# Performance work log

Measured on AMD Instinct MI355X. Metric: run time of the kernel, lower is better.

## Reference

```python
import jax, jax.numpy as jnp
import numpy as np

B, N, C = 2, 2048, 1152
H = 16
HD = C // H  # 72
SCALE = HD ** -0.5
NEG = -100000000.0  # -1e8 bias for fp32 masked positions


def setup_inputs() -> dict:
    key = jax.random.key(0)
    k1, k2, k3, k4, k5 = jax.random.split(key, 5)
    x = jax.random.normal(k1, (B, N, C), dtype=jnp.float32)
    attn_mask = jax.random.randint(k2, (B, N), 0, 2, dtype=jnp.int32)
    w_qkv = jax.random.normal(k3, (3 * C, C), dtype=jnp.float32) * 0.02
    w_proj = jax.random.normal(k4, (C, C), dtype=jnp.float32) * 0.02
    b_proj = jax.random.normal(k5, (C,), dtype=jnp.float32) * 0.02
    return {"x": x, "attn_mask": attn_mask, "w_qkv": w_qkv, "w_proj": w_proj, "b_proj": b_proj}


def reference(x, attn_mask, w_qkv, w_proj, b_proj):
    # qkv projection: [B,N,3C] -> [3,B,H,N,HD]
    qkv = (x @ w_qkv.T).reshape(B, N, 3, H, HD).transpose(2, 0, 3, 1, 4)
    q, k, v = qkv[0], qkv[1], qkv[2]

    # additive mask bias from outer product of per-token 0/1 mask
    m = attn_mask.astype(x.dtype)          # [B,N]
    mm = m[:, :, None] * m[:, None, :]      # [B,N,N]
    bias = jnp.where(mm == 0, NEG, jnp.where(mm == 1, 0.0, mm))
    bias = bias[:, None, :, :]              # [B,1,N,N] broadcast over heads

    # math-branch attention: full QK^T, bias add, softmax, NaN patch, AV
    attn = jnp.einsum('bhqd,bhkd->bhqk', q, k) * SCALE + bias
    attn = jax.nn.softmax(attn, axis=-1)
    attn = jnp.where(jnp.isnan(attn), 0.0, attn)
    out = jnp.einsum('bhqk,bhkd->bqhd', attn, v).reshape(B, N, C)

    return out @ w_proj.T + b_proj
```

## Files before the change

### kernel.cpp

```cpp
#include <hip/hip_runtime.h>

#define B_   2
#define N_   2048
#define C_   1152
#define H_   16
#define HD_  72
#define QKV_W 3456
#define SCALE_ 0.11785113019775793f
#define NEG_  -100000000.0f
#define HDP  96
#define HDV  80
#define PRE_  0.1700219068852255f
#define FMAX_ 4.0f
#define KNEG_ 16384.0f

typedef __bf16    bf16x8 __attribute__((ext_vector_type(8)));
typedef _Float16  f16x8  __attribute__((ext_vector_type(8)));
typedef _Float16  f16x4  __attribute__((ext_vector_type(4)));
typedef float     f32x4  __attribute__((ext_vector_type(4)));

#define GLOAD_LDS16(gp, lp)                                                    \
  __builtin_amdgcn_global_load_lds(                                            \
      (const __attribute__((address_space(1))) void*)(gp),                     \
      (__attribute__((address_space(3))) void*)(lp), 16, 0, 0)

static __device__ __forceinline__ unsigned pack2h(_Float16 a, _Float16 b) {
  union { _Float16 h[2]; unsigned u; } u;
  u.h[0] = a; u.h[1] = b; return u.u;
}

__global__ __launch_bounds__(256)
void split3_f16(const float* __restrict__ x, const float* __restrict__ wq,
                const float* __restrict__ wp,
                _Float16* __restrict__ xf, _Float16* __restrict__ wqf,
                _Float16* __restrict__ wpf,
                float* __restrict__ meanAcc, int nmv,
                int n8x, int n8q, int n8p) {
  int i = blockIdx.x * 256 + threadIdx.x;
  if (i < nmv) meanAcc[i] = 0.0f;
  const float* src; _Float16* dst;
  if (i < n8x) { src = x; dst = xf; }
  else if (i < n8x + n8q) { i -= n8x; src = wq; dst = wqf; }
  else {
    i -= n8x + n8q;
    if (i >= n8p) return;
    src = wp; dst = wpf;
  }
  const float4* p = (const float4*)src + (size_t)i * 2;
  float4 a = p[0], b = p[1];
  float xs[8] = {a.x, a.y, a.z, a.w, b.x, b.y, b.z, b.w};
  f16x8 hv;
#pragma unroll
  for (int r = 0; r < 8; ++r) hv[r] = (_Float16)xs[r];
  *(f16x8*)(dst + (size_t)i * 8) = hv;
}

__global__ __launch_bounds__(256)
void gemm_f16(const _Float16* __restrict__ A, const _Float16* __restrict__ Bm,
              const float* __restrict__ bias, float* __restrict__ Cout,
              int M, int Nn, int K) {
  __shared__ uint4 lds[2][1024];

  const int tid  = threadIdx.x;
  const int wv   = tid >> 6;
  const int lane = tid & 63;
  const int wm   = wv >> 1;
  const int wn   = wv & 1;
  const int m0 = blockIdx.x * 128, n0 = blockIdx.y * 128;

  const char* gp[4];
  int gd[4];
#pragma unroll
  for (int i = 0; i < 4; ++i) {
    const int gid = wv * 4 + i;
    if (gid < 8) {
      gd[i] = gid * 64;
      gp[i] = (const char*)(A + (size_t)(m0 + gid * 16 + (lane & 15)) * K +
                            ((lane >> 4) << 3));
    } else {
      const int g2 = gid - 8;
      gd[i] = 512 + g2 * 64;
      gp[i] = (const char*)(Bm + (size_t)(n0 + g2 * 16 + (lane & 15)) * K +
                            ((lane >> 4) << 3));
    }
  }

#pragma unroll
  for (int i = 0; i < 4; ++i) {
    GLOAD_LDS16(gp[i], &lds[0][gd[i]]);
    gp[i] += 64;
  }

  f32x4 acc[4][4] = {};
  const int nk = K >> 5;

  for (int kt = 0; kt < nk; ++kt) {
    const int cur = kt & 1, nxt = cur ^ 1;
    __syncthreads();

    if (kt < nk - 1) {
#pragma unroll
      for (int i = 0; i < 4; ++i) {
        GLOAD_LDS16(gp[i], &lds[nxt][gd[i]]);
        gp[i] += 64;
      }
    }

    const uint4* cbuf = lds[cur];
    f16x8 af[4], bf[4];
#pragma unroll
    for (int t = 0; t < 4; ++t) {
      af[t] = *(const f16x8*)&cbuf[(wm * 4 + t) * 64 + lane];
      bf[t] = *(const f16x8*)&cbuf[512 + (wn * 4 + t) * 64 + lane];
    }
#pragma unroll
    for (int i = 0; i < 4; ++i)
#pragma unroll
      for (int j = 0; j < 4; ++j)
        acc[i][j] = __builtin_amdgcn_mfma_f32_16x16x32_f16(af[i], bf[j], acc[i][j], 0, 0, 0);
  }

  const int cl = lane & 15, rq = (lane >> 4) << 2;
#pragma unroll
  for (int j = 0; j < 4; ++j) {
    const int col = n0 + (wn * 4 + j) * 16 + cl;
    const float bv = bias ? bias[col] : 0.0f;
#pragma unroll
    for (int i = 0; i < 4; ++i) {
      const int row = m0 + (wm * 4 + i) * 16 + rq;
#pragma unroll
      for (int r = 0; r < 4; ++r)
        Cout[(size_t)(row + r) * Nn + col] = acc[i][j][r] + bv;
    }
  }
}

__global__ __launch_bounds__(256)
void prep_qkv(const float* __restrict__ qkv, const int* __restrict__ mask,
              _Float16* __restrict__ Qf, _Float16* __restrict__ Kf,
              _Float16* __restrict__ Vt, float* __restrict__ meanAcc) {
  const int nt = blockIdx.x, h = blockIdx.y, b = blockIdx.z;
  const int n0 = nt * 64, bh = b * H_ + h, tid = threadIdx.x;
  __shared__ float vls[64][73];

#pragma unroll
  for (int s = 0; s < 2; ++s) {
    const float* src = qkv + (size_t)(b * N_ + n0) * QKV_W + s * C_ + h * HD_;
    _Float16* of = (s == 0 ? Qf : Kf) + ((size_t)bh * N_ + n0) * HDP;
    for (int idx = tid; idx < 64 * 18; idx += 256) {
      const int row = idx / 18, c = idx % 18, d0 = c * 4;
      float4 v = *(const float4*)(src + (size_t)row * QKV_W + d0);
      if (s == 0) { v.x *= PRE_; v.y *= PRE_; v.z *= PRE_; v.w *= PRE_; }
      f16x4 hv;
      hv[0] = (_Float16)v.x; hv[1] = (_Float16)v.y;
      hv[2] = (_Float16)v.z; hv[3] = (_Float16)v.w;
      *(f16x4*)(of + (size_t)row * HDP + d0) = hv;
    }
  }

  for (int idx = tid; idx < 64 * 3; idx += 256) {
    const int row = idx / 3, c3 = idx % 3;
    const int n = n0 + row;
    f16x8 z = {};
    f16x8 qp = z, kp = z;
    if (c3 == 0) {
      qp[0] = (_Float16)1.0f;
      const int kb = (mask[b * N_ + n] != 0);
      kp[0] = (_Float16)(kb ? -FMAX_ : -KNEG_);
    }
    const size_t base = ((size_t)bh * N_ + n) * HDP + 72 + c3 * 8;
    *(f16x8*)(Qf + base) = qp;
    *(f16x8*)(Kf + base) = kp;
  }

  const float* vsrc = qkv + (size_t)(b * N_ + n0) * QKV_W + 2 * C_ + h * HD_;
  for (int idx = tid; idx < 64 * 18; idx += 256) {
    const int row = idx / 18, c = idx % 18, d0 = c * 4;
    float4 v = *(const float4*)(vsrc + (size_t)row * QKV_W + d0);
    vls[row][d0] = v.x; vls[row][d0 + 1] = v.y;
    vls[row][d0 + 2] = v.z; vls[row][d0 + 3] = v.w;
  }
  __syncthreads();
  if (tid < HD_) {
    float sum = 0.0f;
#pragma unroll 8
    for (int r = 0; r < 64; ++r) sum += vls[r][tid];
    atomicAdd(&meanAcc[bh * HD_ + tid], sum);
  }
  for (int idx = tid; idx < HDV * 64; idx += 256) {
    const int d = idx >> 6, nn = idx & 63;
    const float v = (d < HD_) ? vls[nn][d] : 0.0f;
    Vt[((size_t)bh * HDV + d) * N_ + n0 + nn] = (_Float16)v;
  }
}

__global__ __launch_bounds__(256)
void attn_mfma(const _Float16* __restrict__ Qf, const _Float16* __restrict__ Kf,
               const _Float16* __restrict__ Vt, const float* __restrict__ meanV,
               const int* __restrict__ mask, _Float16* __restrict__ att) {
  const int bh = blockIdx.x, qt = blockIdx.y;
  const int b = bh >> 4, h = bh & 15;
  const int tid = threadIdx.x, wv = tid >> 6, lane = tid & 63;
  const int lq = lane & 15;
  const int lg = lane >> 4;
  const int q0 = qt * 64;

  __shared__ uint4 lds[2][22 * 64];
  __shared__ __align__(16) _Float16 Pbuf[4][16][72];

  f16x8 qh[3];
  {
    const size_t qoff = ((size_t)bh * N_ + q0 + wv * 16 + lq) * HDP + lg * 8;
#pragma unroll
    for (int c = 0; c < 3; ++c)
      qh[c] = *(const f16x8*)(Qf + qoff + c * 32);
  }

  const _Float16* kb = Kf + (size_t)bh * N_ * HDP;
  const _Float16* vb = Vt + (size_t)bh * HDV * (size_t)N_;

  const int gstart = (wv < 2) ? wv * 6 : 12 + (wv - 2) * 5;
  const int gcount = (wv < 2) ? 6 : 5;
  const char* gptr[6];
  long gstepB[6];
  int gdst[6];
#pragma unroll
  for (int i = 0; i < 6; ++i) {
    int gid = gstart + i;
    if (gid > 21) gid = 21;
    gdst[i] = gid * 64;
    if (gid < 12) {
      const int tile = gid / 3, ch = gid - tile * 3;
      gptr[i] = (const char*)(kb + (size_t)(tile * 16 + lq) * HDP + ch * 32 + lg * 8);
      gstepB[i] = 64 * HDP * 2;
    } else {
      const int v = gid - 12, td = v >> 1, ck = v & 1;
      gptr[i] = (const char*)(vb + (size_t)(td * 16 + lq) * N_ + ck * 32 + lg * 8);
      gstepB[i] = 64 * 2;
    }
  }

#pragma unroll
  for (int i = 0; i < 6; ++i)
    if (i < gcount) {
      GLOAD_LDS16(gptr[i], &lds[0][gdst[i]]);
      gptr[i] += gstepB[i];
    }

  float l_run = 0.0f;
  f32x4 Oacc[5] = {};

  for (int kt = 0; kt < N_ / 64; ++kt) {
    const int cur = kt & 1, nxt = cur ^ 1;
    __syncthreads();

    if (kt < N_ / 64 - 1) {
#pragma unroll
      for (int i = 0; i < 6; ++i)
        if (i < gcount) {
          GLOAD_LDS16(gptr[i], &lds[nxt][gdst[i]]);
          gptr[i] += gstepB[i];
        }
    }

    const uint4* cbuf = lds[cur];

    f32x4 s[4] = {};
#pragma unroll
    for (int ch = 0; ch < 3; ++ch)
#pragma unroll
      for (int t = 0; t < 4; ++t) {
        f16x8 kf = *(const f16x8*)&cbuf[(t * 3 + ch) * 64 + lane];
        s[t] = __builtin_amdgcn_mfma_f32_16x16x32_f16(kf, qh[ch], s[t], 0, 0, 0);
      }

    float psum = 0.0f;
#pragma unroll
    for (int t = 0; t < 4; ++t) {
      const float p0 = exp2f(s[t][0]);
      const float p1 = exp2f(s[t][1]);
      const float p2 = exp2f(s[t][2]);
      const float p3 = exp2f(s[t][3]);
      psum += (p0 + p1) + (p2 + p3);
      *(uint2*)&Pbuf[wv][lq][t * 16 + 4 * lg] =
          make_uint2(pack2h((_Float16)p0, (_Float16)p1),
                     pack2h((_Float16)p2, (_Float16)p3));
    }
    l_run += psum;

#pragma unroll
    for (int ck = 0; ck < 2; ++ck) {
      f16x8 pf = *(const f16x8*)&Pbuf[wv][lq][ck * 32 + lg * 8];
#pragma unroll
      for (int td = 0; td < 5; ++td) {
        f16x8 vf = *(const f16x8*)&cbuf[(12 + td * 2 + ck) * 64 + lane];
        Oacc[td] = __builtin_amdgcn_mfma_f32_16x16x32_f16(vf, pf, Oacc[td], 0, 0, 0);
      }
    }
  }

  __syncthreads();
  float l = l_run;
  l += __shfl_xor(l, 16);
  l += __shfl_xor(l, 32);
  const float inv = 1.0f / l;

  float* osc = (float*)lds;
  float* myo = osc + wv * 16 * 81;
#pragma unroll
  for (int td = 0; td < 5; ++td)
#pragma unroll
    for (int r = 0; r < 4; ++r)
      myo[lq * 81 + td * 16 + 4 * lg + r] = Oacc[td][r] * inv;
  __syncthreads();

  const int rq = lane >> 2, jj = lane & 3;
  const int q = q0 + wv * 16 + rq;
  const int qm = (mask[b * N_ + q] != 0);
  const float* rowp = myo + rq * 81 + jj * 18;
  const float* mvp  = meanV + bh * HD_ + jj * 18;
  const size_t obase = ((size_t)(b * N_) + q) * C_ + h * HD_ + jj * 18;
#pragma unroll
  for (int e = 0; e < 9; ++e) {
    const float a = qm ? rowp[2 * e]     : mvp[2 * e]     * (1.0f / 2048.0f);
    const float c = qm ? rowp[2 * e + 1] : mvp[2 * e + 1] * (1.0f / 2048.0f);
    *(unsigned*)(att + obase + 2 * e) = pack2h((_Float16)a, (_Float16)c);
  }
}

__global__ __launch_bounds__(256)
void gemm64_nt(const float* __restrict__ A, const float* __restrict__ Bm,
               const float* __restrict__ bias, float* __restrict__ C,
               int M, int N, int K) {
  __shared__ __align__(16) float As[32][68];
  __shared__ __align__(16) float Bs[32][68];
  const int tid = threadIdx.x;
  const int tx = tid & 15, ty = tid >> 4;
  const int m0 = blockIdx.x * 64, n0 = blockIdx.y * 64;
  float acc[4][4] = {};
  for (int k0 = 0; k0 < K; k0 += 32) {
#pragma unroll
    for (int i = 0; i < 2; ++i) {
      const int idx = tid + i * 256;
      const int row = idx >> 3, kc = (idx & 7) << 2;
      float4 a = *(const float4*)(A + (size_t)(m0 + row) * K + k0 + kc);
      As[kc + 0][row] = a.x; As[kc + 1][row] = a.y;
      As[kc + 2][row] = a.z; As[kc + 3][row] = a.w;
      float4 b = *(const float4*)(Bm + (size_t)(n0 + row) * K + k0 + kc);
      Bs[kc + 0][row] = b.x; Bs[kc + 1][row] = b.y;
      Bs[kc + 2][row] = b.z; Bs[kc + 3][row] = b.w;
    }
    __syncthreads();
#pragma unroll
    for (int k = 0; k < 32; ++k) {
      float4 av4 = *(const float4*)&As[k][ty << 2];
      float4 bv4 = *(const float4*)&Bs[k][tx << 2];
      float av[4] = {av4.x, av4.y, av4.z, av4.w};
      float bv[4] = {bv4.x, bv4.y, bv4.z, bv4.w};
#pragma unroll
      for (int i = 0; i < 4; ++i)
#pragma unroll
        for (int j = 0; j < 4; ++j) acc[i][j] += av[i] * bv[j];
    }
    __syncthreads();
  }
#pragma unroll
  for (int i = 0; i < 4; ++i) {
    const int row = m0 + (ty << 2) + i, col = n0 + (tx << 2);
    float4 v = make_float4(acc[i][0], acc[i][1], acc[i][2], acc[i][3]);
    if (bias) {
      v.x += bias[col + 0]; v.y += bias[col + 1];
      v.z += bias[col + 2]; v.w += bias[col + 3];
    }
    *(float4*)(C + (size_t)row * N + col) = v;
  }
}

__global__ __launch_bounds__(256)
void attn_kernel(const float* __restrict__ qkv, const int* __restrict__ mask,
                 float* __restrict__ out) {
  const int qt = blockIdx.x, h = blockIdx.y, b = blockIdx.z;
  const int tid = threadIdx.x;
  const int q0 = qt * 64;
  __shared__ __align__(16) float qT[HD_][68];
  __shared__ __align__(16) float kT[HD_][68];
  __shared__ __align__(16) float vT[HD_][68];
  __shared__ float rowm[64], rowl[64], rowa[64];
  __shared__ float biask[64];
  __shared__ int   mq[64];
  float (*ps)[68] = (float (*)[68])kT;
  const float* qg = qkv + (size_t)(b * N_ + q0) * QKV_W + h * HD_;
  for (int idx = tid; idx < 64 * HD_; idx += 256) {
    const int qi = idx / HD_, d = idx % HD_;
    qT[d][qi] = qg[(size_t)qi * QKV_W + d];
  }
  if (tid < 64) {
    rowm[tid] = -1e30f; rowl[tid] = 0.0f;
    mq[tid] = mask[b * N_ + q0 + tid];
  }
  const int sqg = tid >> 4, skg = tid & 15;
  const int oqg = tid >> 3, ods = tid & 7;
  float o[4][9];
#pragma unroll
  for (int i = 0; i < 4; ++i)
#pragma unroll
    for (int dd = 0; dd < 9; ++dd) o[i][dd] = 0.0f;
  __syncthreads();
  for (int kt = 0; kt < N_ / 64; ++kt) {
    const int k0 = kt * 64;
    const float* kg = qkv + (size_t)(b * N_ + k0) * QKV_W + C_ + h * HD_;
    const float* vg = qkv + (size_t)(b * N_ + k0) * QKV_W + 2 * C_ + h * HD_;
    for (int idx = tid; idx < 64 * HD_; idx += 256) {
      const int kj = idx / HD_, d = idx % HD_;
      kT[d][kj] = kg[(size_t)kj * QKV_W + d];
      vT[d][kj] = vg[(size_t)kj * QKV_W + d];
    }
    if (tid < 64) biask[tid] = (mask[b * N_ + k0 + tid] != 0) ? 0.0f : NEG_;
    __syncthreads();
    float sacc[4][4] = {};
    for (int d = 0; d < HD_; ++d) {
      float4 qv4 = *(const float4*)&qT[d][sqg << 2];
      float4 kv4 = *(const float4*)&kT[d][skg << 2];
      float qa[4] = {qv4.x, qv4.y, qv4.z, qv4.w};
      float ka[4] = {kv4.x, kv4.y, kv4.z, kv4.w};
#pragma unroll
      for (int i = 0; i < 4; ++i)
#pragma unroll
        for (int j = 0; j < 4; ++j) sacc[i][j] += qa[i] * ka[j];
    }
    __syncthreads();
#pragma unroll
    for (int i = 0; i < 4; ++i) {
      const int qi = (sqg << 2) + i;
      const int qm2 = mq[qi];
#pragma unroll
      for (int j = 0; j < 4; ++j) {
        const int kj = (skg << 2) + j;
        const float bias = (qm2 != 0) ? biask[kj] : NEG_;
        ps[qi][kj] = sacc[i][j] * SCALE_ + bias;
      }
    }
    __syncthreads();
    if (tid < 64) {
      float mt = -1e30f;
#pragma unroll
      for (int j4 = 0; j4 < 16; ++j4) {
        float4 p4 = *(const float4*)&ps[tid][j4 << 2];
        mt = fmaxf(mt, fmaxf(fmaxf(p4.x, p4.y), fmaxf(p4.z, p4.w)));
      }
      const float mo = rowm[tid];
      const float nm = fmaxf(mo, mt);
      const float a = __expf(mo - nm);
      float sum = 0.0f;
#pragma unroll
      for (int j4 = 0; j4 < 16; ++j4) {
        float4 p4 = *(const float4*)&ps[tid][j4 << 2];
        p4.x = __expf(p4.x - nm); p4.y = __expf(p4.y - nm);
        p4.z = __expf(p4.z - nm); p4.w = __expf(p4.w - nm);
        sum += p4.x + p4.y + p4.z + p4.w;
        *(float4*)&ps[tid][j4 << 2] = p4;
      }
      rowl[tid] = rowl[tid] * a + sum;
      rowm[tid] = nm;
      rowa[tid] = a;
    }
    __syncthreads();
    if (tid < 128) {
#pragma unroll
      for (int i = 0; i < 4; ++i) {
        const float a = rowa[(oqg << 2) + i];
#pragma unroll
        for (int dd = 0; dd < 9; ++dd) o[i][dd] *= a;
      }
      for (int k4 = 0; k4 < 16; ++k4) {
        float4 pv4[4];
#pragma unroll
        for (int i = 0; i < 4; ++i)
          pv4[i] = *(const float4*)&ps[(oqg << 2) + i][k4 << 2];
        float pa[4][4];
#pragma unroll
        for (int i = 0; i < 4; ++i) {
          pa[i][0] = pv4[i].x; pa[i][1] = pv4[i].y;
          pa[i][2] = pv4[i].z; pa[i][3] = pv4[i].w;
        }
#pragma unroll
        for (int dd = 0; dd < 9; ++dd) {
          float4 vv4 = *(const float4*)&vT[ods * 9 + dd][k4 << 2];
          float va[4] = {vv4.x, vv4.y, vv4.z, vv4.w};
#pragma unroll
          for (int i = 0; i < 4; ++i)
            o[i][dd] += pa[i][0] * va[0] + pa[i][1] * va[1] +
                        pa[i][2] * va[2] + pa[i][3] * va[3];
        }
      }
    }
    __syncthreads();
  }
  if (tid < 128) {
#pragma unroll
    for (int i = 0; i < 4; ++i) {
      const int qi = (oqg << 2) + i;
      const float inv = 1.0f / rowl[qi];
      const size_t base = (size_t)(b * N_ + q0 + qi) * C_ + h * HD_ + ods * 9;
#pragma unroll
      for (int dd = 0; dd < 9; ++dd) out[base + dd] = o[i][dd] * inv;
    }
  }
}

extern "C" void kernel_launch(void* const* d_in, const int* in_sizes, int n_in,
                              void* d_out, int out_size, void* d_ws, size_t ws_size,
                              hipStream_t stream) {
  (void)in_sizes; (void)n_in; (void)out_size;

  const float* x      = (const float*)d_in[0];
  const int*   mask   = (const int*)  d_in[1];
  const float* w_qkv  = (const float*)d_in[2];
  const float* w_proj = (const float*)d_in[3];
  const float* b_proj = (const float*)d_in[4];
  float* out = (float*)d_out;

  const size_t XE = (size_t)B_ * N_ * C_;
  const size_t WQ = (size_t)QKV_W * C_;
  const size_t WP = (size_t)C_ * C_;
  const size_t QKVE = (size_t)B_ * N_ * QKV_W;
  const size_t QKE  = (size_t)B_ * H_ * N_ * HDP;
  const size_t VTE  = (size_t)B_ * H_ * HDV * N_;
  const int    MVN  = B_ * H_ * HD_;

  char* w = (char*)d_ws;
  float*    qkv = (float*)w;
  _Float16* att = (_Float16*)w;
  char* A0 = w + QKVE * 4;
  _Float16* x_f  = (_Float16*)A0;
  _Float16* wq_f = x_f + XE;
  _Float16* wp_f = wq_f + WQ;
  _Float16* Qf   = wp_f + WP;
  _Float16* Kf   = Qf + QKE;
  _Float16* Vt   = Kf + QKE;
  float* meanAcc = (float*)(Vt + VTE);
  const size_t need = (size_t)((char*)(meanAcc + MVN) - w);

  if (ws_size >= need) {
    const int n8x = (int)(XE / 8), n8q = (int)(WQ / 8), n8p = (int)(WP / 8);
    const int nblk = (n8x + n8q + n8p + 255) / 256;
    split3_f16<<<nblk, 256, 0, stream>>>(x, w_qkv, w_proj, x_f, wq_f, wp_f,
                                         meanAcc, MVN, n8x, n8q, n8p);

    gemm_f16<<<dim3(32, 27), 256, 0, stream>>>(x_f, wq_f, nullptr, qkv,
                                               B_ * N_, QKV_W, C_);
    prep_qkv<<<dim3(32, 16, 2), 256, 0, stream>>>(qkv, mask, Qf, Kf, Vt, meanAcc);

    attn_mfma<<<dim3(32, 32), 256, 0, stream>>>(Qf, Kf, Vt, meanAcc, mask, att);

    gemm_f16<<<dim3(32, 9), 256, 0, stream>>>(att, wp_f, b_proj, out,
                                              B_ * N_, C_, C_);
  } else {
    float* qkv_f = (float*)d_ws;
    float* att_f = qkv_f + QKVE;
    gemm64_nt<<<dim3(64, 54), 256, 0, stream>>>(x, w_qkv, nullptr, qkv_f,
                                                B_ * N_, QKV_W, C_);
    attn_kernel<<<dim3(32, 16, 2), 256, 0, stream>>>(qkv_f, mask, att_f);
    gemm64_nt<<<dim3(64, 18), 256, 0, stream>>>(att_f, w_proj, b_proj, out,
                                                B_ * N_, C_, C_);
  }
}
```

Baseline: 328.3 us.

## Process two 64-query blocks per attention workgroup to reuse K/V tiles

Each attention workgroup now handles 128 queries instead of 64, holding two sets of Q fragments, score tiles, P buffers and output accumulators. Each K/V tile loaded into LDS is used for twice as many MFMAs, halving global K/V traffic and the number of loads per query. The grid drops from 1024 to 512 workgroups, and register and LDS use per wave roughly doubles, which can lower occupancy and leave fewer blocks to fill the CUs.

Measured after the change: 298.2 us. -9.2%, faster.

```diff
diff --git a/kernel.cpp b/kernel.cpp
--- a/kernel.cpp
+++ b/kernel.cpp
@@ -203,17 +203,19 @@
   const int tid = threadIdx.x, wv = tid >> 6, lane = tid & 63;
   const int lq = lane & 15;
   const int lg = lane >> 4;
-  const int q0 = qt * 64;
+  const int q0 = qt * 128;
 
   __shared__ uint4 lds[2][22 * 64];
-  __shared__ __align__(16) _Float16 Pbuf[4][16][72];
-
-  f16x8 qh[3];
-  {
-    const size_t qoff = ((size_t)bh * N_ + q0 + wv * 16 + lq) * HDP + lg * 8;
+  __shared__ __align__(16) _Float16 Pbuf[2][4][16][72];
+
+  f16x8 qh[2][3];
+#pragma unroll
+  for (int bd = 0; bd < 2; ++bd) {
+    const size_t qoff =
+        ((size_t)bh * N_ + q0 + bd * 64 + wv * 16 + lq) * HDP + lg * 8;
 #pragma unroll
     for (int c = 0; c < 3; ++c)
-      qh[c] = *(const f16x8*)(Qf + qoff + c * 32);
+      qh[bd][c] = *(const f16x8*)(Qf + qoff + c * 32);
   }
 
   const _Float16* kb = Kf + (size_t)bh * N_ * HDP;
@@ -247,8 +249,8 @@
       gptr[i] += gstepB[i];
     }
 
-  float l_run = 0.0f;
-  f32x4 Oacc[5] = {};
+  float l_run[2] = {0.0f, 0.0f};
+  f32x4 Oacc[2][5] = {};
 
   for (int kt = 0; kt < N_ / 64; ++kt) {
     const int cur = kt & 1, nxt = cur ^ 1;
@@ -265,66 +267,76 @@
 
     const uint4* cbuf = lds[cur];
 
-    f32x4 s[4] = {};
+    f32x4 s[2][4] = {};
 #pragma unroll
     for (int ch = 0; ch < 3; ++ch)
 #pragma unroll
       for (int t = 0; t < 4; ++t) {
         f16x8 kf = *(const f16x8*)&cbuf[(t * 3 + ch) * 64 + lane];
-        s[t] = __builtin_amdgcn_mfma_f32_16x16x32_f16(kf, qh[ch], s[t], 0, 0, 0);
-      }
-
-    float psum = 0.0f;
-#pragma unroll
-    for (int t = 0; t < 4; ++t) {
-      const float p0 = exp2f(s[t][0]);
-      const float p1 = exp2f(s[t][1]);
-      const float p2 = exp2f(s[t][2]);
-      const float p3 = exp2f(s[t][3]);
-      psum += (p0 + p1) + (p2 + p3);
-      *(uint2*)&Pbuf[wv][lq][t * 16 + 4 * lg] =
-          make_uint2(pack2h((_Float16)p0, (_Float16)p1),
-                     pack2h((_Float16)p2, (_Float16)p3));
-    }
-    l_run += psum;
+        s[0][t] = __builtin_amdgcn_mfma_f32_16x16x32_f16(kf, qh[0][ch], s[0][t], 0, 0, 0);
+        s[1][t] = __builtin_amdgcn_mfma_f32_16x16x32_f16(kf, qh[1][ch], s[1][t], 0, 0, 0);
+      }
+
+#pragma unroll
+    for (int bd = 0; bd < 2; ++bd) {
+      float psum = 0.0f;
+#pragma unroll
+      for (int t = 0; t < 4; ++t) {
+        const float p0 = exp2f(s[bd][t][0]);
+        const float p1 = exp2f(s[bd][t][1]);
+        const float p2 = exp2f(s[bd][t][2]);
+        const float p3 = exp2f(s[bd][t][3]);
+        psum += (p0 + p1) + (p2 + p3);
+        *(uint2*)&Pbuf[bd][wv][lq][t * 16 + 4 * lg] =
+            make_uint2(pack2h((_Float16)p0, (_Float16)p1),
+                       pack2h((_Float16)p2, (_Float16)p3));
+      }
+      l_run[bd] += psum;
+    }
 
 #pragma unroll
     for (int ck = 0; ck < 2; ++ck) {
-      f16x8 pf = *(const f16x8*)&Pbuf[wv][lq][ck * 32 + lg * 8];
+      f16x8 pf0 = *(const f16x8*)&Pbuf[0][wv][lq][ck * 32 + lg * 8];
+      f16x8 pf1 = *(const f16x8*)&Pbuf[1][wv][lq][ck * 32 + lg * 8];
 #pragma unroll
       for (int td = 0; td < 5; ++td) {
         f16x8 vf = *(const f16x8*)&cbuf[(12 + td * 2 + ck) * 64 + lane];
-        Oacc[td] = __builtin_amdgcn_mfma_f32_16x16x32_f16(vf, pf, Oacc[td], 0, 0, 0);
+        Oacc[0][td] = __builtin_amdgcn_mfma_f32_16x16x32_f16(vf, pf0, Oacc[0][td], 0, 0, 0);
+        Oacc[1][td] = __builtin_amdgcn_mfma_f32_16x16x32_f16(vf, pf1, Oacc[1][td], 0, 0, 0);
       }
     }
   }
 
   __syncthreads();
-  float l = l_run;
-  l += __shfl_xor(l, 16);
-  l += __shfl_xor(l, 32);
-  const float inv = 1.0f / l;
-
   float* osc = (float*)lds;
   float* myo = osc + wv * 16 * 81;
-#pragma unroll
-  for (int td = 0; td < 5; ++td)
-#pragma unroll
-    for (int r = 0; r < 4; ++r)
-      myo[lq * 81 + td * 16 + 4 * lg + r] = Oacc[td][r] * inv;
-  __syncthreads();
-
   const int rq = lane >> 2, jj = lane & 3;
-  const int q = q0 + wv * 16 + rq;
-  const int qm = (mask[b * N_ + q] != 0);
-  const float* rowp = myo + rq * 81 + jj * 18;
-  const float* mvp  = meanV + bh * HD_ + jj * 18;
-  const size_t obase = ((size_t)(b * N_) + q) * C_ + h * HD_ + jj * 18;
-#pragma unroll
-  for (int e = 0; e < 9; ++e) {
-    const float a = qm ? rowp[2 * e]     : mvp[2 * e]     * (1.0f / 2048.0f);
-    const float c = qm ? rowp[2 * e + 1] : mvp[2 * e + 1] * (1.0f / 2048.0f);
-    *(unsigned*)(att + obase + 2 * e) = pack2h((_Float16)a, (_Float16)c);
+
+#pragma unroll
+  for (int bd = 0; bd < 2; ++bd) {
+    float l = l_run[bd];
+    l += __shfl_xor(l, 16);
+    l += __shfl_xor(l, 32);
+    const float inv = 1.0f / l;
+#pragma unroll
+    for (int td = 0; td < 5; ++td)
+#pragma unroll
+      for (int r = 0; r < 4; ++r)
+        myo[lq * 81 + td * 16 + 4 * lg + r] = Oacc[bd][td][r] * inv;
+    __syncthreads();
+
+    const int q = q0 + bd * 64 + wv * 16 + rq;
+    const int qm = (mask[b * N_ + q] != 0);
+    const float* rowp = myo + rq * 81 + jj * 18;
+    const float* mvp  = meanV + bh * HD_ + jj * 18;
+    const size_t obase = ((size_t)(b * N_) + q) * C_ + h * HD_ + jj * 18;
+#pragma unroll
+    for (int e = 0; e < 9; ++e) {
+      const float a = qm ? rowp[2 * e]     : mvp[2 * e]     * (1.0f / 2048.0f);
+      const float c = qm ? rowp[2 * e + 1] : mvp[2 * e + 1] * (1.0f / 2048.0f);
+      *(unsigned*)(att + obase + 2 * e) = pack2h((_Float16)a, (_Float16)c);
+    }
+    __syncthreads();
   }
 }
 
@@ -551,7 +563,7 @@
                                                B_ * N_, QKV_W, C_);
     prep_qkv<<<dim3(32, 16, 2), 256, 0, stream>>>(qkv, mask, Qf, Kf, Vt, meanAcc);
 
-    attn_mfma<<<dim3(32, 32), 256, 0, stream>>>(Qf, Kf, Vt, meanAcc, mask, att);
+    attn_mfma<<<dim3(32, 16), 256, 0, stream>>>(Qf, Kf, Vt, meanAcc, mask, att);
 
     gemm_f16<<<dim3(32, 9), 256, 0, stream>>>(att, wp_f, b_proj, out,
                                               B_ * N_, C_, C_);
```
